# Kernel tuning notes

Hardware: AMD Instinct MI355X
Metric: run time of the kernel (lower is better)

The kernel has to match this reference:

```python
import jax, jax.numpy as jnp
import numpy as np

N_NODES = 100000
HIDDEN = 128
E = 524288  # edges per graph (pos and neg)


def setup_inputs() -> dict:
    key = jax.random.key(0)
    ks = jax.random.split(key, 8)
    return {
        "z_src": jax.random.normal(ks[0], (N_NODES, HIDDEN), dtype=jnp.float32),
        "z_dst": jax.random.normal(ks[1], (N_NODES, HIDDEN), dtype=jnp.float32),
        "pos_src": jax.random.randint(ks[2], (E,), 0, N_NODES, dtype=jnp.int64),
        "pos_dst": jax.random.randint(ks[3], (E,), 0, N_NODES, dtype=jnp.int64),
        "neg_src": jax.random.randint(ks[4], (E,), 0, N_NODES, dtype=jnp.int64),
        "neg_dst": jax.random.randint(ks[5], (E,), 0, N_NODES, dtype=jnp.int64),
        "W1": jax.random.normal(ks[6], (2 * HIDDEN, HIDDEN), dtype=jnp.float32) * (1.0 / np.sqrt(2 * HIDDEN)),
        "b1": jnp.zeros((HIDDEN,), dtype=jnp.float32),
        "W2": jax.random.normal(ks[7], (HIDDEN, 1), dtype=jnp.float32) * (1.0 / np.sqrt(HIDDEN)),
        "b2": jnp.zeros((1,), dtype=jnp.float32),
    }


def reference(z_src, z_dst, pos_src, pos_dst, neg_src, neg_dst, W1, b1, W2, b2):
    # Gather endpoint features for pos then neg edges (cat along edge dim)
    src_idx = jnp.concatenate([pos_src, neg_src])  # [2E]
    dst_idx = jnp.concatenate([pos_dst, neg_dst])  # [2E]
    z = jnp.concatenate([z_src[src_idx], z_dst[dst_idx]], axis=-1)  # [2E, 2h]
    z = jax.nn.relu(z @ W1 + b1)  # [2E, h]
    z = z @ W2 + b2               # [2E, 1]
    return z.reshape(-1)
```

## Files before the change

### kernel.cpp

```cpp
#include <hip/hip_runtime.h>
#include <hip/hip_bf16.h>
#include <cstdint>

#define N_NODES 100000
#define HIDDEN  128
#define NEDGE   524288

typedef __attribute__((ext_vector_type(8))) short short8;
typedef __attribute__((ext_vector_type(4))) float f32x4;

__device__ __forceinline__ unsigned short f2b(float f) {
    unsigned u = __float_as_uint(f);
    u += 0x7FFFu + ((u >> 16) & 1u);
    return (unsigned short)(u >> 16);
}
__device__ __forceinline__ float b2f(unsigned x16) {
    return __uint_as_float(x16 << 16);
}

__global__ void wt_kernel(const float* __restrict__ W1,
                          unsigned short* __restrict__ Wt)
{
    const int row = blockIdx.x;
    const int n = row & 127;
    const int tb = row >> 7;
    const int k = threadIdx.x;
    Wt[(size_t)row * 128 + k] = f2b(W1[(size_t)(tb * 128 + k) * 128 + n]);
}

__global__ __launch_bounds__(256, 4)
void precompute_kernel(const float* __restrict__ z_src,
                       const float* __restrict__ z_dst,
                       const unsigned short* __restrict__ Wt,
                       unsigned short* __restrict__ Asrc,
                       unsigned short* __restrict__ Adst)
{
    const int table = blockIdx.y;
    const float* z = table ? z_dst : z_src;
    const unsigned short* W = Wt + table * (128 * 128);
    unsigned short* A = table ? Adst : Asrc;

    const int wave = threadIdx.x >> 6;
    const int lane = threadIdx.x & 63;
    const int t = lane & 15;
    const int q = lane >> 4;

    const int m0 = (blockIdx.x * 4 + wave) * 16;
    if (m0 >= N_NODES) return;

    const float* zrow = z + (size_t)(m0 + t) * 128;

    f32x4 acc[8];
#pragma unroll
    for (int n = 0; n < 8; ++n) acc[n] = (f32x4){0.f, 0.f, 0.f, 0.f};

#pragma unroll
    for (int ks = 0; ks < 4; ++ks) {
        const int k0 = ks * 32 + q * 8;
        const float4 v0 = *(const float4*)(zrow + k0);
        const float4 v1 = *(const float4*)(zrow + k0 + 4);
        short8 b;
        b[0] = (short)f2b(v0.x); b[1] = (short)f2b(v0.y);
        b[2] = (short)f2b(v0.z); b[3] = (short)f2b(v0.w);
        b[4] = (short)f2b(v1.x); b[5] = (short)f2b(v1.y);
        b[6] = (short)f2b(v1.z); b[7] = (short)f2b(v1.w);
#pragma unroll
        for (int n = 0; n < 8; ++n) {
            const short8 a = *(const short8*)(W + (size_t)(n * 16 + t) * 128 + k0);
            acc[n] = __builtin_amdgcn_mfma_f32_16x16x32_bf16(a, b, acc[n], 0, 0, 0);
        }
    }

    unsigned short* arow = A + (size_t)(m0 + t) * 128;
#pragma unroll
    for (int n = 0; n < 8; ++n) {
        ushort4 h;
        h.x = f2b(acc[n][0]); h.y = f2b(acc[n][1]);
        h.z = f2b(acc[n][2]); h.w = f2b(acc[n][3]);
        *(ushort4*)(arow + n * 16 + q * 4) = h;
    }
}

__global__ __launch_bounds__(256, 4)
void edge_kernel(const unsigned short* __restrict__ Asrc,
                 const unsigned short* __restrict__ Adst,
                 const int* __restrict__ pos_src,
                 const int* __restrict__ pos_dst,
                 const int* __restrict__ neg_src,
                 const int* __restrict__ neg_dst,
                 const float* __restrict__ b1,
                 const float* __restrict__ W2,
                 const float* __restrict__ b2,
                 float* __restrict__ out)
{
    const int tid = threadIdx.x;
    const int t = tid & 15;
    const int g = tid >> 4;

    const bool is_pos = blockIdx.x < 4096;
    const int* __restrict__ sp = is_pos ? pos_src : neg_src;
    const int* __restrict__ dp = is_pos ? pos_dst : neg_dst;
    const int eb = (is_pos ? blockIdx.x : blockIdx.x - 4096) * 128;

    float b1r[8], w2r[8];
#pragma unroll
    for (int j = 0; j < 8; ++j) {
        b1r[j] = b1[t * 8 + j];
        w2r[j] = W2[t * 8 + j];
    }
    const float bias2 = b2[0];

    int sidx[8], didx[8];
#pragma unroll
    for (int i = 0; i < 8; ++i) {
        sidx[i] = sp[eb + i * 16 + g];
        didx[i] = dp[eb + i * 16 + g];
    }

    uint4 ua[8], ub[8];
#pragma unroll
    for (int i = 0; i < 8; ++i) {
        ua[i] = *(const uint4*)(Asrc + (size_t)sidx[i] * 128 + t * 8);
        ub[i] = *(const uint4*)(Adst + (size_t)didx[i] * 128 + t * 8);
    }

#pragma unroll
    for (int i = 0; i < 8; ++i) {
        float acc = 0.f;
        const unsigned* pa = (const unsigned*)&ua[i];
        const unsigned* pb = (const unsigned*)&ub[i];
#pragma unroll
        for (int j2 = 0; j2 < 4; ++j2) {
            float h0 = b2f(pa[j2] & 0xFFFFu) + b2f(pb[j2] & 0xFFFFu) + b1r[2 * j2];
            float h1 = b2f(pa[j2] >> 16)     + b2f(pb[j2] >> 16)     + b1r[2 * j2 + 1];
            h0 = fmaxf(h0, 0.f);
            h1 = fmaxf(h1, 0.f);
            acc = fmaf(h0, w2r[2 * j2], acc);
            acc = fmaf(h1, w2r[2 * j2 + 1], acc);
        }
        acc += __shfl_xor(acc, 1);
        acc += __shfl_xor(acc, 2);
        acc += __shfl_xor(acc, 4);
        acc += __shfl_xor(acc, 8);
        if (t == 0) out[blockIdx.x * 128 + i * 16 + g] = acc + bias2;
    }
}

extern "C" void kernel_launch(void* const* d_in, const int* in_sizes, int n_in,
                              void* d_out, int out_size, void* d_ws, size_t ws_size,
                              hipStream_t stream) {
    const float* z_src  = (const float*)d_in[0];
    const float* z_dst  = (const float*)d_in[1];
    const int* pos_src  = (const int*)d_in[2];
    const int* pos_dst  = (const int*)d_in[3];
    const int* neg_src  = (const int*)d_in[4];
    const int* neg_dst  = (const int*)d_in[5];
    const float* W1     = (const float*)d_in[6];
    const float* b1     = (const float*)d_in[7];
    const float* W2     = (const float*)d_in[8];
    const float* b2     = (const float*)d_in[9];
    float* out = (float*)d_out;

    unsigned short* Asrc = (unsigned short*)d_ws;
    unsigned short* Adst = Asrc + (size_t)N_NODES * HIDDEN;
    unsigned short* Wt   = Adst + (size_t)N_NODES * HIDDEN;

    wt_kernel<<<256, 128, 0, stream>>>(W1, Wt);

    dim3 pgrid(1563, 2);
    precompute_kernel<<<pgrid, 256, 0, stream>>>(z_src, z_dst, Wt, Asrc, Adst);

    edge_kernel<<<8192, 256, 0, stream>>>(Asrc, Adst, pos_src, pos_dst,
                                          neg_src, neg_dst, b1, W2, b2, out);
}
```

Before: 258.7 us.

## Make precompute kernel persistent with LDS-staged weights and prefetched rows

The precompute GEMM kernel becomes a grid-stride persistent kernel with 391 blocks per table. Each block stages the bf16 weight fragments once into shared memory, so the weights are no longer re-read from global memory for every 16-row tile. It also software-prefetches the next tile's z rows while running MFMAs on the current tile. This adds 32KB of LDS per block, more register pressure and fewer blocks, which may reduce latency hiding in a kernel that is mostly bound by memory bandwidth.

New measurement: 272.2 us. 1.05x slower.

```diff
diff --git a/kernel.cpp b/kernel.cpp
--- a/kernel.cpp
+++ b/kernel.cpp
@@ -5,6 +5,8 @@
 #define N_NODES 100000
 #define HIDDEN  128
 #define NEDGE   524288
+#define NTILES  1563
+#define PGRIDX  391
 
 typedef __attribute__((ext_vector_type(8))) short short8;
 typedef __attribute__((ext_vector_type(4))) float f32x4;
@@ -28,7 +30,7 @@
     Wt[(size_t)row * 128 + k] = f2b(W1[(size_t)(tb * 128 + k) * 128 + n]);
 }
 
-__global__ __launch_bounds__(256, 4)
+__global__ __launch_bounds__(256, 3)
 void precompute_kernel(const float* __restrict__ z_src,
                        const float* __restrict__ z_dst,
                        const unsigned short* __restrict__ Wt,
@@ -40,44 +42,88 @@
     const unsigned short* W = Wt + table * (128 * 128);
     unsigned short* A = table ? Adst : Asrc;
 
-    const int wave = threadIdx.x >> 6;
-    const int lane = threadIdx.x & 63;
+    __shared__ unsigned short fragbuf[32 * 64 * 8];
+
+    const int tid = threadIdx.x;
+#pragma unroll
+    for (int i = 0; i < 8; ++i) {
+        const int f = tid + i * 256;
+        const int nks = f >> 6;
+        const int n = nks >> 2, ks = nks & 3;
+        const int qq = (f >> 4) & 3, tt = f & 15;
+        const short8 v = *(const short8*)(W + ((n * 16 + tt) * 128 + ks * 32 + qq * 8));
+        *(short8*)&fragbuf[f * 8] = v;
+    }
+    __syncthreads();
+
+    const int wave = tid >> 6;
+    const int lane = tid & 63;
     const int t = lane & 15;
     const int q = lane >> 4;
 
-    const int m0 = (blockIdx.x * 4 + wave) * 16;
-    if (m0 >= N_NODES) return;
-
-    const float* zrow = z + (size_t)(m0 + t) * 128;
-
-    f32x4 acc[8];
-#pragma unroll
-    for (int n = 0; n < 8; ++n) acc[n] = (f32x4){0.f, 0.f, 0.f, 0.f};
-
-#pragma unroll
-    for (int ks = 0; ks < 4; ++ks) {
-        const int k0 = ks * 32 + q * 8;
-        const float4 v0 = *(const float4*)(zrow + k0);
-        const float4 v1 = *(const float4*)(zrow + k0 + 4);
-        short8 b;
-        b[0] = (short)f2b(v0.x); b[1] = (short)f2b(v0.y);
-        b[2] = (short)f2b(v0.z); b[3] = (short)f2b(v0.w);
-        b[4] = (short)f2b(v1.x); b[5] = (short)f2b(v1.y);
-        b[6] = (short)f2b(v1.z); b[7] = (short)f2b(v1.w);
+    float4 s[8];
+    int tile = blockIdx.x;
+    {
+        const int row = tile * 64 + wave * 16 + t;
+        const bool ok = row < N_NODES;
+        const float* zrow = z + (size_t)row * 128;
+        const float4 zv = make_float4(0.f, 0.f, 0.f, 0.f);
+#pragma unroll
+        for (int ks = 0; ks < 4; ++ks) {
+            s[2 * ks]     = ok ? *(const float4*)(zrow + ks * 32 + q * 8)     : zv;
+            s[2 * ks + 1] = ok ? *(const float4*)(zrow + ks * 32 + q * 8 + 4) : zv;
+        }
+    }
+
+    while (tile < NTILES) {
+        const int row = tile * 64 + wave * 16 + t;
+        const bool ok = row < N_NODES;
+
+        short8 b[4];
+#pragma unroll
+        for (int ks = 0; ks < 4; ++ks) {
+            const float4 v0 = s[2 * ks], v1 = s[2 * ks + 1];
+            b[ks][0] = (short)f2b(v0.x); b[ks][1] = (short)f2b(v0.y);
+            b[ks][2] = (short)f2b(v0.z); b[ks][3] = (short)f2b(v0.w);
+            b[ks][4] = (short)f2b(v1.x); b[ks][5] = (short)f2b(v1.y);
+            b[ks][6] = (short)f2b(v1.z); b[ks][7] = (short)f2b(v1.w);
+        }
+
+        const int next = tile + PGRIDX;
+        if (next < NTILES) {
+            const int nrow = next * 64 + wave * 16 + t;
+            const bool nok = nrow < N_NODES;
+            const float* zrow = z + (size_t)nrow * 128;
+            const float4 zv = make_float4(0.f, 0.f, 0.f, 0.f);
+#pragma unroll
+            for (int ks = 0; ks < 4; ++ks) {
+                s[2 * ks]     = nok ? *(const float4*)(zrow + ks * 32 + q * 8)     : zv;
+                s[2 * ks + 1] = nok ? *(const float4*)(zrow + ks * 32 + q * 8 + 4) : zv;
+            }
+        }
+
+        f32x4 acc[8];
+#pragma unroll
+        for (int n = 0; n < 8; ++n) acc[n] = (f32x4){0.f, 0.f, 0.f, 0.f};
+
 #pragma unroll
         for (int n = 0; n < 8; ++n) {
-            const short8 a = *(const short8*)(W + (size_t)(n * 16 + t) * 128 + k0);
-            acc[n] = __builtin_amdgcn_mfma_f32_16x16x32_bf16(a, b, acc[n], 0, 0, 0);
-        }
-    }
-
-    unsigned short* arow = A + (size_t)(m0 + t) * 128;
-#pragma unroll
-    for (int n = 0; n < 8; ++n) {
-        ushort4 h;
-        h.x = f2b(acc[n][0]); h.y = f2b(acc[n][1]);
-        h.z = f2b(acc[n][2]); h.w = f2b(acc[n][3]);
-        *(ushort4*)(arow + n * 16 + q * 4) = h;
+#pragma unroll
+            for (int ks = 0; ks < 4; ++ks) {
+                const short8 a = *(const short8*)&fragbuf[((n * 4 + ks) * 64 + lane) * 8];
+                acc[n] = __builtin_amdgcn_mfma_f32_16x16x32_bf16(a, b[ks], acc[n], 0, 0, 0);
+            }
+        }
+
+        unsigned short* arow = A + (size_t)row * 128;
+#pragma unroll
+        for (int n = 0; n < 8; ++n) {
+            ushort4 h;
+            h.x = f2b(acc[n][0]); h.y = f2b(acc[n][1]);
+            h.z = f2b(acc[n][2]); h.w = f2b(acc[n][3]);
+            if (ok) *(ushort4*)(arow + n * 16 + q * 4) = h;
+        }
+        tile = next;
     }
 }
 
@@ -167,7 +213,7 @@
 
     wt_kernel<<<256, 128, 0, stream>>>(W1, Wt);
 
-    dim3 pgrid(1563, 2);
+    dim3 pgrid(PGRIDX, 2);
     precompute_kernel<<<pgrid, 256, 0, stream>>>(z_src, z_dst, Wt, Asrc, Adst);
 
     edge_kernel<<<8192, 256, 0, stream>>>(Asrc, Adst, pos_src, pos_dst,
```

## Make precompute persistent with register-resident W and async LDS double-buffering

Applied to the files above, without the earlier changes.

Turns the node-projection kernel into a persistent grid-stride kernel. Each wave keeps the whole bf16 W fragment set in registers, prepacked by a new wp kernel into MFMA lane order. z tiles are double-buffered into swizzled LDS with global_load_lds async copies, so the load of the next tile overlaps the MFMAs on the current one. The goal is to stop re-reading W from global memory for every tile and to hide z load latency. The cost is heavy register pressure (32 short8 fragments) and fewer resident blocks, with launch bounds lowered to 2.

Result: faster. 222.4 us (-14.0%).

```diff
diff --git a/kernel.cpp b/kernel.cpp
--- a/kernel.cpp
+++ b/kernel.cpp
@@ -5,6 +5,9 @@
 #define N_NODES 100000
 #define HIDDEN  128
 #define NEDGE   524288
+#define NT      6250
+#define PBLK    256
+#define WSTRIDE (PBLK * 4)
 
 typedef __attribute__((ext_vector_type(8))) short short8;
 typedef __attribute__((ext_vector_type(4))) float f32x4;
@@ -18,67 +21,119 @@
     return __uint_as_float(x16 << 16);
 }
 
-__global__ void wt_kernel(const float* __restrict__ W1,
-                          unsigned short* __restrict__ Wt)
+__device__ __forceinline__ void async_copy16(const float* g, float* l) {
+    __builtin_amdgcn_global_load_lds(
+        (const __attribute__((address_space(1))) unsigned int*)g,
+        (__attribute__((address_space(3))) unsigned int*)l,
+        16, 0, 0);
+}
+
+__global__ void wp_kernel(const float* __restrict__ W1,
+                          unsigned short* __restrict__ Wp)
 {
-    const int row = blockIdx.x;
-    const int n = row & 127;
-    const int tb = row >> 7;
-    const int k = threadIdx.x;
-    Wt[(size_t)row * 128 + k] = f2b(W1[(size_t)(tb * 128 + k) * 128 + n]);
-}
-
-__global__ __launch_bounds__(256, 4)
+    const int f = blockIdx.x;
+    const int tb = blockIdx.y;
+    const int lane = threadIdx.x;
+    const int t = lane & 15, q = lane >> 4;
+    const int n = f >> 2, ks = f & 3;
+    short8 v;
+#pragma unroll
+    for (int j = 0; j < 8; ++j)
+        v[j] = (short)f2b(W1[(size_t)(tb * 128 + ks * 32 + q * 8 + j) * 128 + n * 16 + t]);
+    *(short8*)(Wp + ((size_t)(tb * 32 + f) * 64 + lane) * 8) = v;
+}
+
+__global__ __launch_bounds__(256, 2)
 void precompute_kernel(const float* __restrict__ z_src,
                        const float* __restrict__ z_dst,
-                       const unsigned short* __restrict__ Wt,
+                       const unsigned short* __restrict__ Wp,
                        unsigned short* __restrict__ Asrc,
                        unsigned short* __restrict__ Adst)
 {
     const int table = blockIdx.y;
-    const float* z = table ? z_dst : z_src;
-    const unsigned short* W = Wt + table * (128 * 128);
-    unsigned short* A = table ? Adst : Asrc;
-
-    const int wave = threadIdx.x >> 6;
-    const int lane = threadIdx.x & 63;
+    const float* __restrict__ z = table ? z_dst : z_src;
+    unsigned short* __restrict__ A = table ? Adst : Asrc;
+
+    __shared__ float zbuf[4][2][2048];
+
+    const int tid = threadIdx.x;
+    const int wave = tid >> 6;
+    const int lane = tid & 63;
     const int t = lane & 15;
     const int q = lane >> 4;
 
-    const int m0 = (blockIdx.x * 4 + wave) * 16;
-    if (m0 >= N_NODES) return;
-
-    const float* zrow = z + (size_t)(m0 + t) * 128;
-
-    f32x4 acc[8];
-#pragma unroll
-    for (int n = 0; n < 8; ++n) acc[n] = (f32x4){0.f, 0.f, 0.f, 0.f};
-
-#pragma unroll
-    for (int ks = 0; ks < 4; ++ks) {
-        const int k0 = ks * 32 + q * 8;
-        const float4 v0 = *(const float4*)(zrow + k0);
-        const float4 v1 = *(const float4*)(zrow + k0 + 4);
-        short8 b;
-        b[0] = (short)f2b(v0.x); b[1] = (short)f2b(v0.y);
-        b[2] = (short)f2b(v0.z); b[3] = (short)f2b(v0.w);
-        b[4] = (short)f2b(v1.x); b[5] = (short)f2b(v1.y);
-        b[6] = (short)f2b(v1.z); b[7] = (short)f2b(v1.w);
+    short8 wfrag[32];
+    {
+        const unsigned short* wp = Wp + ((size_t)table * 32 * 64 + lane) * 8;
+#pragma unroll
+        for (int f = 0; f < 32; ++f)
+            wfrag[f] = *(const short8*)(wp + (size_t)f * 64 * 8);
+    }
+
+    const int lhi = lane >> 5;
+    const int llo = lane & 31;
+#define STAGE(m0, p)                                                          \
+    do {                                                                      \
+        _Pragma("unroll")                                                     \
+        for (int j = 0; j < 8; ++j) {                                         \
+            const int r = j * 2 + lhi;                                        \
+            const int c = llo ^ (r & 7);                                      \
+            async_copy16(z + (size_t)((m0) + r) * 128 + c * 4,                \
+                         &zbuf[wave][p][j * 256]);                            \
+        }                                                                     \
+    } while (0)
+
+    int tile = blockIdx.x * 4 + wave;
+    int p = 0;
+    STAGE(tile * 16, 0);
+    __builtin_amdgcn_s_waitcnt(0xF70);
+    asm volatile("" ::: "memory");
+
+    while (tile < NT) {
+        const int m0 = tile * 16;
+        const int ntile = tile + WSTRIDE;
+        const int nm0 = (ntile < NT ? ntile : tile) * 16;
+        STAGE(nm0, p ^ 1);
+        asm volatile("" ::: "memory");
+        __builtin_amdgcn_s_waitcnt(0xF78);
+        asm volatile("" ::: "memory");
+
+        short8 b[4];
+#pragma unroll
+        for (int ks = 0; ks < 4; ++ks) {
+            const int c0 = ks * 8 + 2 * q;
+            const int s = t & 7;
+            const float4 v0 = *(const float4*)&zbuf[wave][p][(t * 32 + (c0 ^ s)) * 4];
+            const float4 v1 = *(const float4*)&zbuf[wave][p][(t * 32 + ((c0 + 1) ^ s)) * 4];
+            b[ks][0] = (short)f2b(v0.x); b[ks][1] = (short)f2b(v0.y);
+            b[ks][2] = (short)f2b(v0.z); b[ks][3] = (short)f2b(v0.w);
+            b[ks][4] = (short)f2b(v1.x); b[ks][5] = (short)f2b(v1.y);
+            b[ks][6] = (short)f2b(v1.z); b[ks][7] = (short)f2b(v1.w);
+        }
+
+        f32x4 acc[8];
+#pragma unroll
+        for (int n = 0; n < 8; ++n) acc[n] = (f32x4){0.f, 0.f, 0.f, 0.f};
+#pragma unroll
+        for (int n = 0; n < 8; ++n)
+#pragma unroll
+            for (int ks = 0; ks < 4; ++ks)
+                acc[n] = __builtin_amdgcn_mfma_f32_16x16x32_bf16(
+                             wfrag[n * 4 + ks], b[ks], acc[n], 0, 0, 0);
+
+        unsigned short* arow = A + (size_t)(m0 + t) * 128;
 #pragma unroll
         for (int n = 0; n < 8; ++n) {
-            const short8 a = *(const short8*)(W + (size_t)(n * 16 + t) * 128 + k0);
-            acc[n] = __builtin_amdgcn_mfma_f32_16x16x32_bf16(a, b, acc[n], 0, 0, 0);
+            ushort4 h;
+            h.x = f2b(acc[n][0]); h.y = f2b(acc[n][1]);
+            h.z = f2b(acc[n][2]); h.w = f2b(acc[n][3]);
+            *(ushort4*)(arow + n * 16 + q * 4) = h;
         }
-    }
-
-    unsigned short* arow = A + (size_t)(m0 + t) * 128;
-#pragma unroll
-    for (int n = 0; n < 8; ++n) {
-        ushort4 h;
-        h.x = f2b(acc[n][0]); h.y = f2b(acc[n][1]);
-        h.z = f2b(acc[n][2]); h.w = f2b(acc[n][3]);
-        *(ushort4*)(arow + n * 16 + q * 4) = h;
-    }
+
+        p ^= 1;
+        tile = ntile;
+    }
+#undef STAGE
 }
 
 __global__ __launch_bounds__(256, 4)
@@ -163,12 +218,12 @@
 
     unsigned short* Asrc = (unsigned short*)d_ws;
     unsigned short* Adst = Asrc + (size_t)N_NODES * HIDDEN;
-    unsigned short* Wt   = Adst + (size_t)N_NODES * HIDDEN;
-
-    wt_kernel<<<256, 128, 0, stream>>>(W1, Wt);
-
-    dim3 pgrid(1563, 2);
-    precompute_kernel<<<pgrid, 256, 0, stream>>>(z_src, z_dst, Wt, Asrc, Adst);
+    unsigned short* Wp   = Adst + (size_t)N_NODES * HIDDEN;
+
+    wp_kernel<<<dim3(32, 2), 64, 0, stream>>>(W1, Wp);
+
+    precompute_kernel<<<dim3(PBLK, 2), 256, 0, stream>>>(z_src, z_dst, Wp,
+                                                         Asrc, Adst);
 
     edge_kernel<<<8192, 256, 0, stream>>>(Asrc, Adst, pos_src, pos_dst,
                                           neg_src, neg_dst, b1, W2, b2, out);
```
